# Optimization experiments

Hardware: AMD Instinct MI355X
Metric: run time of the kernel (lower is better)

Reference implementation:

```python
import jax, jax.numpy as jnp
import numpy as np

TAU_RC = 0.02
TAU_REF = 0.002
V_TH = 1.0
EPS = 1e-7


def lif_rate(I):
    # LIF firing-rate nonlinearity: r = 1/(tau_ref - tau_rc*log1p(-v_th/I)) for I > v_th+eps else 0
    good = I > V_TH + EPS
    safe_I = jnp.where(good, I, V_TH + 1.0)  # avoid log1p of invalid values
    r = 1.0 / (TAU_REF - TAU_RC * jnp.log1p(-V_TH / safe_I))
    return jnp.where(good, r, 0.0)


def setup_inputs() -> dict:
    key = jax.random.key(0)
    kq, kk, kv, ke, kg, kb = jax.random.split(key, 6)
    B, H, T, D = 2, 16, 2048, 64
    block_size = 2048
    Q = jax.random.normal(kq, (B, H, T, D), dtype=jnp.float32)
    K = jax.random.normal(kk, (B, H, T, D), dtype=jnp.float32)
    V = jax.random.normal(kv, (B, H, T, D), dtype=jnp.float32)
    enc = jax.random.normal(ke, (H, block_size, D), dtype=jnp.float32)
    # F.normalize(enc, dim=-1, eps=1e-8): x / max(||x||, eps)
    norm = jnp.maximum(jnp.linalg.norm(enc, axis=-1, keepdims=True), 1e-8)
    enc_hat = enc / norm
    gain = jax.random.uniform(kg, (1, H, block_size, 1), dtype=jnp.float32) * 200.0
    bias = jax.random.uniform(kb, (1, H, block_size, 1), dtype=jnp.float32)
    return {"Q": Q, "K": K, "V": V, "enc_hat": enc_hat, "gain": gain, "bias": bias}


def reference(Q, K, V, enc_hat, gain, bias):
    B, H, T, D = Q.shape
    temperature = jnp.asarray(D ** 0.5, dtype=Q.dtype)
    E = enc_hat[:, :T, :]          # [H, T, D]
    G = gain[:, :, :T, :]          # [1, H, T, 1]
    BIAS = bias[:, :, :T, :]       # [1, H, T, 1]
    # scores against fixed encoders (K is unused, matching the original module)
    I = G * jnp.einsum('bhtd,hsd->bhts', Q, E) + BIAS   # [B, H, T, T]
    scores = lif_rate(I) / temperature
    causal = jnp.tril(jnp.ones((T, T), dtype=bool))[None, None]
    scores = jnp.where(causal, scores, -jnp.inf)
    attn = jax.nn.softmax(scores, axis=-1)
    return jnp.einsum('bhts,bhsd->bhtd', attn, V)
```

## Files before the change

### kernel.cpp

```cpp
#include <hip/hip_runtime.h>
#include <hip/hip_bf16.h>
#include <math.h>

constexpr int Bb = 2, Hh = 16, Tt = 2048;

typedef __attribute__((ext_vector_type(8))) _Float16 f16x8;
typedef __attribute__((ext_vector_type(8))) short bf16x8;
typedef __attribute__((ext_vector_type(4))) float f32x4;
typedef __attribute__((ext_vector_type(16))) float f32x16;
typedef __attribute__((ext_vector_type(4))) unsigned int u32x4;
typedef unsigned int u32;

__device__ __forceinline__ short f2bf(float x){ __hip_bfloat16 h = __float2bfloat16(x); return *(short*)&h; }
__device__ __forceinline__ int swze(int row, int e){ return row*64 + ((((e>>3) ^ (row&7))<<3) | (e&7)); }
__device__ __forceinline__ int swzg(int row, int e0){ return row*64 + ((((e0>>3) ^ (row&7))<<3)); }

__device__ __forceinline__ void gll16(const void* g, void* l){
  __builtin_amdgcn_global_load_lds((const __attribute__((address_space(1))) u32*)g,
                                   (__attribute__((address_space(3))) u32*)l, 16, 0, 0);
}
__device__ __forceinline__ u32 cvtpk(float lo, float hi){
  u32 d; asm("v_cvt_pk_bf16_f32 %0, %1, %2" : "=v"(d) : "v"(lo), "v"(hi)); return d;
}

__global__ __launch_bounds__(256) void prep_e(const float* __restrict__ E, char* __restrict__ Eimg){
  const float* src = E + (size_t)blockIdx.x * 4096;
  char* dst = Eimg + (size_t)blockIdx.x * 16384;
#pragma unroll
  for (int i = 0; i < 2; ++i) {
    const int gid = threadIdx.x + 256 * i;
    const int row = gid >> 3, gc = gid & 7;
    const float* s8 = src + row * 64 + gc * 8;
    float4 a = *(const float4*)s8;
    float4 c = *(const float4*)(s8 + 4);
    float v[8] = {a.x, a.y, a.z, a.w, c.x, c.y, c.z, c.w};
    f16x8 hv, lv;
#pragma unroll
    for (int k = 0; k < 8; ++k) {
      _Float16 hi = (_Float16)v[k];
      hv[k] = hi; lv[k] = (_Float16)(v[k] - (float)hi);
    }
    const int off = row * 128 + ((gc ^ (row & 7)) << 4);
    *(f16x8*)(dst + off) = hv;
    *(f16x8*)(dst + 8192 + off) = lv;
  }
}

__global__ __launch_bounds__(256) void prep_v(const float* __restrict__ V, char* __restrict__ Vimg){
  __shared__ __align__(16) short Tl[64 * 64];
  const int tid = threadIdx.x;
  const int j = blockIdx.x & 31, bh = blockIdx.x >> 5;
  const int s0 = j * 64;
  {
    const int r = tid >> 2, c0 = (tid & 3) * 16;
    const float* src = V + ((size_t)bh * Tt + s0 + r) * 64 + c0;
#pragma unroll
    for (int i = 0; i < 4; ++i) {
      float4 t4 = ((const float4*)src)[i];
      float vv[4] = {t4.x, t4.y, t4.z, t4.w};
#pragma unroll
      for (int k = 0; k < 4; ++k) Tl[swze(c0 + 4 * i + k, r)] = f2bf(vv[k]);
    }
  }
  __syncthreads();
  {
    const int d = tid >> 2, sg = (tid & 3) * 16;
    bf16x8 a = *(const bf16x8*)&Tl[swzg(d, sg)];
    bf16x8 b = *(const bf16x8*)&Tl[swzg(d, sg + 8)];
    char* dst = Vimg + (size_t)blockIdx.x * 8192;
    *(bf16x8*)(dst + (sg >> 3) * 1024 + d * 16)       = a;
    *(bf16x8*)(dst + ((sg >> 3) + 1) * 1024 + d * 16) = b;
  }
}

__global__ __launch_bounds__(256, 3) void lif_attn15(
    const float* __restrict__ Q, const float* __restrict__ gain, const float* __restrict__ bias,
    const char* __restrict__ Eimg, const char* __restrict__ Vimg, float* __restrict__ out)
{
  __shared__ __align__(16) char Eb[2][16384];
  __shared__ __align__(16) float LsS[128];

  const int tid = threadIdx.x, lane = tid & 63;
  const int l31 = lane & 31, hi2 = lane >> 5;
  const int w = tid >> 6, wc = w & 1, wr = w >> 1;
  const int bh = blockIdx.x & 31, tb = 31 - (blockIdx.x >> 5);
  const int b = bh >> 4, h = bh & 15, t0 = tb * 64;
  const int tg = t0 + 32 * wc + l31;

  const char* etile = Eimg + (size_t)(h * 32) * 16384;
  const char* vtile = Vimg + (size_t)(bh * 32) * 8192;

  f16x8 qh[4], ql[4];
  {
    const float* qp = Q + ((size_t)(b * Hh + h) * Tt + tg) * 64 + 8 * hi2;
#pragma unroll
    for (int kk = 0; kk < 4; ++kk) {
      const float* p0 = qp + 16 * kk;
      float4 a = *(const float4*)p0;
      float4 c = *(const float4*)(p0 + 4);
      float v[8] = {a.x, a.y, a.z, a.w, c.x, c.y, c.z, c.w};
#pragma unroll
      for (int k = 0; k < 8; ++k) {
        _Float16 hi = (_Float16)v[k];
        qh[kk][k] = hi; ql[kk][k] = (_Float16)(v[k] - (float)hi);
      }
    }
  }
  const float gt = gain[h * Tt + tg], bt = bias[h * Tt + tg];

  const int rS = 32 * wr + l31;
  const int eB = rS * 128 + ((hi2 ^ (rS & 7)) << 4);

  const int g8a = 4 * wr + hi2;
  const char* vp0 = vtile + g8a * 1024 + l31 * 16;
  const char* vp1 = vtile + g8a * 1024 + (32 + l31) * 16;
  const char* vp2 = vtile + (g8a + 2) * 1024 + l31 * 16;
  const char* vp3 = vtile + (g8a + 2) * 1024 + (32 + l31) * 16;

  f32x16 oacc0 = 0.f, oacc1 = 0.f;
  float lsum = 0.f;
  f32x16 sA, sB;
  bf16x8 vA[4], vB[4];

  auto STAGE_E = [&](int n, int buf) {
    const char* g = etile + (size_t)n * 16384 + tid * 16;
    char* l = &Eb[buf][0] + tid * 16;
#pragma unroll
    for (int c2 = 0; c2 < 4; ++c2) gll16(g + c2 * 4096, l + c2 * 4096);
  };
  auto SSTEP = [&](int buf, f32x16& acc) {
    const char* ec = &Eb[buf][0];
    acc = 0.f;
#pragma unroll
    for (int kk = 0; kk < 4; ++kk) {
      f16x8 eh = *(const f16x8*)(ec + (eB ^ (kk << 5)));
      f16x8 el = *(const f16x8*)(ec + 8192 + (eB ^ (kk << 5)));
      acc = __builtin_amdgcn_mfma_f32_32x32x16_f16(eh, qh[kk], acc, 0, 0, 0);
      acc = __builtin_amdgcn_mfma_f32_32x32x16_f16(el, qh[kk], acc, 0, 0, 0);
      acc = __builtin_amdgcn_mfma_f32_32x32x16_f16(eh, ql[kk], acc, 0, 0, 0);
    }
  };
  auto VLOAD = [&](int n, bf16x8* vv) {
    const size_t o = (size_t)n * 8192;
    vv[0] = *(const bf16x8*)(vp0 + o);
    vv[1] = *(const bf16x8*)(vp1 + o);
    vv[2] = *(const bf16x8*)(vp2 + o);
    vv[3] = *(const bf16x8*)(vp3 + o);
  };

  auto BODY = [&](int j, f32x16& cur, f32x16& nxt, bf16x8* vc, bf16x8* vn) {
    if (j + 2 <= tb) STAGE_E(j + 2, j & 1);
    __builtin_amdgcn_sched_barrier(0);
    if (j + 1 <= tb) { SSTEP((j + 1) & 1, nxt); VLOAD(j + 1, vn); }
    float p[16];
#pragma unroll
    for (int r = 0; r < 16; ++r) {
      const float I = fmaf(gt, cur[r], bt);
      const float a = (I - 1.0f) * __builtin_fabsf(__builtin_amdgcn_rcpf(I));
      const float L2 = __log2f(a);
      const float den = fmaf(-0.013862944f, L2, 0.002f);
      const float rd = __builtin_amdgcn_rcpf(den);
      const float pv = __builtin_amdgcn_exp2f(fmaf(0.18033688f, rd, -90.169312f));
      p[r] = fmaxf(pv, 7.1892351e-28f);
    }
    if (j == tb) {
#pragma unroll
      for (int rq = 0; rq < 4; ++rq)
#pragma unroll
        for (int rr = 0; rr < 4; ++rr)
          if (32 * wr + 8 * rq + 4 * hi2 + rr > 32 * wc + l31) p[4 * rq + rr] = 0.f;
    }
#pragma unroll
    for (int r = 0; r < 16; ++r) lsum += p[r];
#pragma unroll
    for (int kp = 0; kp < 2; ++kp) {
      u32 x0 = cvtpk(p[8 * kp + 0], p[8 * kp + 1]);
      u32 x1 = cvtpk(p[8 * kp + 2], p[8 * kp + 3]);
      u32 y0 = cvtpk(p[8 * kp + 4], p[8 * kp + 5]);
      u32 y1 = cvtpk(p[8 * kp + 6], p[8 * kp + 7]);
      asm("v_permlane32_swap_b32 %0, %1" : "+v"(x0), "+v"(y0));
      asm("v_permlane32_swap_b32 %0, %1" : "+v"(x1), "+v"(y1));
      u32x4 af = {x0, x1, y0, y1};
      bf16x8 pa = *(bf16x8*)&af;
      oacc0 = __builtin_amdgcn_mfma_f32_32x32x16_bf16(pa, vc[2 * kp + 0], oacc0, 0, 0, 0);
      oacc1 = __builtin_amdgcn_mfma_f32_32x32x16_bf16(pa, vc[2 * kp + 1], oacc1, 0, 0, 0);
    }
  };

  STAGE_E(0, 0);
  if (tb >= 1) STAGE_E(1, 1);
  __builtin_amdgcn_sched_barrier(0);
  VLOAD(0, vA);
  asm volatile("s_waitcnt vmcnt(4)" ::: "memory");
  __builtin_amdgcn_s_barrier();
  __builtin_amdgcn_sched_barrier(0);
  SSTEP(0, sA);
  asm volatile("s_waitcnt vmcnt(4)" ::: "memory");
  __builtin_amdgcn_s_barrier();
  __builtin_amdgcn_sched_barrier(0);

  int j = 0;
  for (;;) {
    BODY(j, sA, sB, vA, vB);
    if (j == tb) break;
    asm volatile("s_waitcnt vmcnt(4)" ::: "memory");
    __builtin_amdgcn_s_barrier();
    __builtin_amdgcn_sched_barrier(0);
    ++j;
    BODY(j, sB, sA, vB, vA);
    if (j == tb) break;
    asm volatile("s_waitcnt vmcnt(4)" ::: "memory");
    __builtin_amdgcn_s_barrier();
    __builtin_amdgcn_sched_barrier(0);
    ++j;
  }

  lsum += __shfl_xor(lsum, 32);
  if (lane < 32) LsS[wr * 64 + wc * 32 + l31] = lsum;
  __syncthreads();
  float* red = (float*)&Eb[0][0];
  if (wr == 1) {
#pragma unroll
    for (int rq = 0; rq < 4; ++rq)
#pragma unroll
      for (int rr = 0; rr < 4; ++rr) {
        const int tr = 8 * rq + 4 * hi2 + rr;
        red[wc * 2048 + tr * 64 + l31]      = oacc0[4 * rq + rr];
        red[wc * 2048 + tr * 64 + 32 + l31] = oacc1[4 * rq + rr];
      }
  }
  __syncthreads();
  if (wr == 0) {
    float* ob = out + ((size_t)(b * Hh + h) * Tt + t0 + 32 * wc) * 64;
#pragma unroll
    for (int rq = 0; rq < 4; ++rq) {
      const int tr0 = 8 * rq + 4 * hi2;
      f32x4 lt0 = *(const f32x4*)&LsS[wc * 32 + tr0];
      f32x4 lt1 = *(const f32x4*)&LsS[64 + wc * 32 + tr0];
#pragma unroll
      for (int rr = 0; rr < 4; ++rr) {
        const int tr = tr0 + rr;
        const float linv = __builtin_amdgcn_rcpf(lt0[rr] + lt1[rr]);
        const float o0 = oacc0[4 * rq + rr] + red[wc * 2048 + tr * 64 + l31];
        const float o1 = oacc1[4 * rq + rr] + red[wc * 2048 + tr * 64 + 32 + l31];
        ob[(size_t)tr * 64 + l31]      = o0 * linv;
        ob[(size_t)tr * 64 + 32 + l31] = o1 * linv;
      }
    }
  }
}

extern "C" void kernel_launch(void* const* d_in, const int* in_sizes, int n_in,
                              void* d_out, int out_size, void* d_ws, size_t ws_size,
                              hipStream_t stream) {
  const float* Q    = (const float*)d_in[0];
  const float* V    = (const float*)d_in[2];
  const float* E    = (const float*)d_in[3];
  const float* gain = (const float*)d_in[4];
  const float* bias = (const float*)d_in[5];
  float* out = (float*)d_out;

  constexpr size_t EIMG_BYTES = (size_t)Hh * 32 * 16384;
  char* Eimg = (char*)d_ws;
  char* Vimg = (char*)d_ws + EIMG_BYTES;

  prep_e<<<Hh * 32, 256, 0, stream>>>(E, Eimg);
  prep_v<<<Bb * Hh * 32, 256, 0, stream>>>(V, Vimg);
  lif_attn15<<<1024, 256, 0, stream>>>(Q, gain, bias, Eimg, Vimg, out);
}
```

Baseline: 72.39 us.

## Split long causal rows across blocks to balance work, then merge partials

Adds a load-balanced causal attention kernel. Each of the 1024 blocks now handles either a long query tile's first 16 key tiles (writing partial output and row sums to workspace), or a pair made of that long tile's remaining key tiles plus a short query tile. A finalize kernel then adds the partials and normalises. This evens out per-block work under the triangular causal mask, at the cost of an extra kernel launch, extra global traffic for partials, and a fallback when the workspace is too small.

Result: slower. 136.0 us (+87.9%).

```diff
diff --git a/kernel.cpp b/kernel.cpp
--- a/kernel.cpp
+++ b/kernel.cpp
@@ -73,6 +73,231 @@
   }
 }
 
+__global__ __launch_bounds__(256, 3) void lif_attn16(
+    const float* __restrict__ Q, const float* __restrict__ gain, const float* __restrict__ bias,
+    const char* __restrict__ Eimg, const char* __restrict__ Vimg, float* __restrict__ out,
+    float* __restrict__ wsAO, float* __restrict__ wsAL, float* __restrict__ wsBL)
+{
+  __shared__ __align__(16) char Eb[2][16384];
+  __shared__ __align__(16) float LsS[128];
+
+  const int tid = threadIdx.x, lane = tid & 63;
+  const int l31 = lane & 31, hi2 = lane >> 5;
+  const int w = tid >> 6, wc = w & 1, wr = w >> 1;
+  const int bh = blockIdx.x & 31;
+  const int m  = blockIdx.x >> 5;
+  const int p  = m & 15, isB = m >> 4;
+  const int b = bh >> 4, h = bh & 15;
+
+  const char* etile = Eimg + (size_t)(h * 32) * 16384;
+  const char* vtile = Vimg + (size_t)(bh * 32) * 8192;
+
+  const int rS = 32 * wr + l31;
+  const int eB = rS * 128 + ((hi2 ^ (rS & 7)) << 4);
+  const int g8a = 4 * wr + hi2;
+  const char* vp0 = vtile + g8a * 1024 + l31 * 16;
+  const char* vp1 = vtile + g8a * 1024 + (32 + l31) * 16;
+  const char* vp2 = vtile + (g8a + 2) * 1024 + l31 * 16;
+  const char* vp3 = vtile + (g8a + 2) * 1024 + (32 + l31) * 16;
+
+  const int nph = 1 + isB;
+  for (int ph = 0; ph < nph; ++ph) {
+    const int tb   = ph ? p : (31 - p);
+    const int jlo  = (isB && ph == 0) ? 16 : 0;
+    const int jhi  = isB ? tb : 15;
+    const int mode = isB ? (ph == 0 ? 1 : 0) : 2;
+    const int t0 = tb * 64;
+    const int tg = t0 + 32 * wc + l31;
+
+    f16x8 qh[4], ql[4];
+    {
+      const float* qp = Q + ((size_t)(b * Hh + h) * Tt + tg) * 64 + 8 * hi2;
+#pragma unroll
+      for (int kk = 0; kk < 4; ++kk) {
+        const float* p0 = qp + 16 * kk;
+        float4 a = *(const float4*)p0;
+        float4 c = *(const float4*)(p0 + 4);
+        float v[8] = {a.x, a.y, a.z, a.w, c.x, c.y, c.z, c.w};
+#pragma unroll
+        for (int k = 0; k < 8; ++k) {
+          _Float16 hi = (_Float16)v[k];
+          qh[kk][k] = hi; ql[kk][k] = (_Float16)(v[k] - (float)hi);
+        }
+      }
+    }
+    const float gt = gain[h * Tt + tg], bt = bias[h * Tt + tg];
+
+    f32x16 oacc0 = 0.f, oacc1 = 0.f;
+    float lsum = 0.f;
+    f32x16 sA, sB;
+    bf16x8 vA[4], vB[4];
+
+    auto STAGE_E = [&](int n) {
+      const char* g = etile + (size_t)n * 16384 + tid * 16;
+      char* l = &Eb[n & 1][0] + tid * 16;
+#pragma unroll
+      for (int c2 = 0; c2 < 4; ++c2) gll16(g + c2 * 4096, l + c2 * 4096);
+    };
+    auto SSTEP = [&](int n, f32x16& acc) {
+      const char* ec = &Eb[n & 1][0];
+      acc = 0.f;
+#pragma unroll
+      for (int kk = 0; kk < 4; ++kk) {
+        f16x8 eh = *(const f16x8*)(ec + (eB ^ (kk << 5)));
+        f16x8 el = *(const f16x8*)(ec + 8192 + (eB ^ (kk << 5)));
+        acc = __builtin_amdgcn_mfma_f32_32x32x16_f16(eh, qh[kk], acc, 0, 0, 0);
+        acc = __builtin_amdgcn_mfma_f32_32x32x16_f16(el, qh[kk], acc, 0, 0, 0);
+        acc = __builtin_amdgcn_mfma_f32_32x32x16_f16(eh, ql[kk], acc, 0, 0, 0);
+      }
+    };
+    auto VLOAD = [&](int n, bf16x8* vv) {
+      const size_t o = (size_t)n * 8192;
+      vv[0] = *(const bf16x8*)(vp0 + o);
+      vv[1] = *(const bf16x8*)(vp1 + o);
+      vv[2] = *(const bf16x8*)(vp2 + o);
+      vv[3] = *(const bf16x8*)(vp3 + o);
+    };
+
+    auto BODY = [&](int j, f32x16& cur, f32x16& nxt, bf16x8* vc, bf16x8* vn) {
+      if (j + 2 <= jhi) STAGE_E(j + 2);
+      __builtin_amdgcn_sched_barrier(0);
+      if (j + 1 <= jhi) { SSTEP(j + 1, nxt); VLOAD(j + 1, vn); }
+      float pp[16];
+#pragma unroll
+      for (int r = 0; r < 16; ++r) {
+        const float I = fmaf(gt, cur[r], bt);
+        const float a = (I - 1.0f) * __builtin_fabsf(__builtin_amdgcn_rcpf(I));
+        const float L2 = __log2f(a);
+        const float den = fmaf(-0.013862944f, L2, 0.002f);
+        const float rd = __builtin_amdgcn_rcpf(den);
+        const float pv = __builtin_amdgcn_exp2f(fmaf(0.18033688f, rd, -90.169312f));
+        pp[r] = fmaxf(pv, 7.1892351e-28f);
+      }
+      if (j == tb) {
+#pragma unroll
+        for (int rq = 0; rq < 4; ++rq)
+#pragma unroll
+          for (int rr = 0; rr < 4; ++rr)
+            if (32 * wr + 8 * rq + 4 * hi2 + rr > 32 * wc + l31) pp[4 * rq + rr] = 0.f;
+      }
+#pragma unroll
+      for (int r = 0; r < 16; ++r) lsum += pp[r];
+#pragma unroll
+      for (int kp = 0; kp < 2; ++kp) {
+        u32 x0 = cvtpk(pp[8 * kp + 0], pp[8 * kp + 1]);
+        u32 x1 = cvtpk(pp[8 * kp + 2], pp[8 * kp + 3]);
+        u32 y0 = cvtpk(pp[8 * kp + 4], pp[8 * kp + 5]);
+        u32 y1 = cvtpk(pp[8 * kp + 6], pp[8 * kp + 7]);
+        asm("v_permlane32_swap_b32 %0, %1" : "+v"(x0), "+v"(y0));
+        asm("v_permlane32_swap_b32 %0, %1" : "+v"(x1), "+v"(y1));
+        u32x4 af = {x0, x1, y0, y1};
+        bf16x8 pa = *(bf16x8*)&af;
+        oacc0 = __builtin_amdgcn_mfma_f32_32x32x16_bf16(pa, vc[2 * kp + 0], oacc0, 0, 0, 0);
+        oacc1 = __builtin_amdgcn_mfma_f32_32x32x16_bf16(pa, vc[2 * kp + 1], oacc1, 0, 0, 0);
+      }
+    };
+
+    STAGE_E(jlo);
+    if (jlo + 1 <= jhi) STAGE_E(jlo + 1);
+    __builtin_amdgcn_sched_barrier(0);
+    VLOAD(jlo, vA);
+    asm volatile("s_waitcnt vmcnt(4)" ::: "memory");
+    __builtin_amdgcn_s_barrier();
+    __builtin_amdgcn_sched_barrier(0);
+    SSTEP(jlo, sA);
+    asm volatile("s_waitcnt vmcnt(4)" ::: "memory");
+    __builtin_amdgcn_s_barrier();
+    __builtin_amdgcn_sched_barrier(0);
+
+    int j = jlo;
+    for (;;) {
+      BODY(j, sA, sB, vA, vB);
+      if (j == jhi) break;
+      asm volatile("s_waitcnt vmcnt(4)" ::: "memory");
+      __builtin_amdgcn_s_barrier();
+      __builtin_amdgcn_sched_barrier(0);
+      ++j;
+      BODY(j, sB, sA, vB, vA);
+      if (j == jhi) break;
+      asm volatile("s_waitcnt vmcnt(4)" ::: "memory");
+      __builtin_amdgcn_s_barrier();
+      __builtin_amdgcn_sched_barrier(0);
+      ++j;
+    }
+
+    lsum += __shfl_xor(lsum, 32);
+    if (lane < 32) LsS[wr * 64 + wc * 32 + l31] = lsum;
+    __syncthreads();
+    float* red = (float*)&Eb[0][0];
+    if (wr == 1) {
+#pragma unroll
+      for (int rq = 0; rq < 4; ++rq)
+#pragma unroll
+        for (int rr = 0; rr < 4; ++rr) {
+          const int tr = 8 * rq + 4 * hi2 + rr;
+          red[wc * 2048 + tr * 64 + l31]      = oacc0[4 * rq + rr];
+          red[wc * 2048 + tr * 64 + 32 + l31] = oacc1[4 * rq + rr];
+        }
+    }
+    __syncthreads();
+    if (wr == 0) {
+      float* ob = out + ((size_t)(b * Hh + h) * Tt + t0 + 32 * wc) * 64;
+      float* ab = wsAO + (size_t)(bh * 16 + p) * 4096 + (size_t)(32 * wc) * 64;
+      float* lb = (mode == 1 ? wsBL : wsAL) + (size_t)(bh * 16 + p) * 64 + 32 * wc;
+#pragma unroll
+      for (int rq = 0; rq < 4; ++rq) {
+        const int tr0 = 8 * rq + 4 * hi2;
+        f32x4 lt0 = *(const f32x4*)&LsS[wc * 32 + tr0];
+        f32x4 lt1 = *(const f32x4*)&LsS[64 + wc * 32 + tr0];
+#pragma unroll
+        for (int rr = 0; rr < 4; ++rr) {
+          const int tr = tr0 + rr;
+          const float lt = lt0[rr] + lt1[rr];
+          const float o0 = oacc0[4 * rq + rr] + red[wc * 2048 + tr * 64 + l31];
+          const float o1 = oacc1[4 * rq + rr] + red[wc * 2048 + tr * 64 + 32 + l31];
+          if (mode == 0) {
+            const float linv = __builtin_amdgcn_rcpf(lt);
+            ob[(size_t)tr * 64 + l31]      = o0 * linv;
+            ob[(size_t)tr * 64 + 32 + l31] = o1 * linv;
+          } else if (mode == 1) {
+            ob[(size_t)tr * 64 + l31]      = o0;
+            ob[(size_t)tr * 64 + 32 + l31] = o1;
+            if (l31 == 0) lb[tr] = lt;
+          } else {
+            ab[(size_t)tr * 64 + l31]      = o0;
+            ab[(size_t)tr * 64 + 32 + l31] = o1;
+            if (l31 == 0) lb[tr] = lt;
+          }
+        }
+      }
+    }
+    __syncthreads();
+  }
+}
+
+__global__ __launch_bounds__(256) void finalize_split(
+    float* __restrict__ out, const float* __restrict__ wsAO,
+    const float* __restrict__ wsAL, const float* __restrict__ wsBL)
+{
+  const int bid = blockIdx.x;
+  const int bh = bid >> 4, p = bid & 15;
+  const int tb = 31 - p, t0 = tb * 64;
+  const int tid = threadIdx.x;
+  const int r = tid >> 2, c0 = (tid & 3) * 16;
+  const float l = wsAL[(size_t)(bh * 16 + p) * 64 + r] + wsBL[(size_t)(bh * 16 + p) * 64 + r];
+  const float linv = __builtin_amdgcn_rcpf(l);
+  float* orow = out + ((size_t)bh * Tt + t0 + r) * 64 + c0;
+  const float* arow = wsAO + (size_t)(bh * 16 + p) * 4096 + (size_t)r * 64 + c0;
+#pragma unroll
+  for (int i = 0; i < 4; ++i) {
+    float4 o = ((float4*)orow)[i];
+    float4 a = ((const float4*)arow)[i];
+    o.x = (o.x + a.x) * linv; o.y = (o.y + a.y) * linv;
+    o.z = (o.z + a.z) * linv; o.w = (o.w + a.w) * linv;
+    ((float4*)orow)[i] = o;
+  }
+}
+
 __global__ __launch_bounds__(256, 3) void lif_attn15(
     const float* __restrict__ Q, const float* __restrict__ gain, const float* __restrict__ bias,
     const char* __restrict__ Eimg, const char* __restrict__ Vimg, float* __restrict__ out)
@@ -107,10 +332,8 @@
     }
   }
   const float gt = gain[h * Tt + tg], bt = bias[h * Tt + tg];
-
   const int rS = 32 * wr + l31;
   const int eB = rS * 128 + ((hi2 ^ (rS & 7)) << 4);
-
   const int g8a = 4 * wr + hi2;
   const char* vp0 = vtile + g8a * 1024 + l31 * 16;
   const char* vp1 = vtile + g8a * 1024 + (32 + l31) * 16;
@@ -147,7 +370,6 @@
     vv[2] = *(const bf16x8*)(vp2 + o);
     vv[3] = *(const bf16x8*)(vp3 + o);
   };
-
   auto BODY = [&](int j, f32x16& cur, f32x16& nxt, bf16x8* vc, bf16x8* vn) {
     if (j + 2 <= tb) STAGE_E(j + 2, j & 1);
     __builtin_amdgcn_sched_barrier(0);
@@ -260,11 +482,24 @@
   const float* bias = (const float*)d_in[5];
   float* out = (float*)d_out;
 
-  constexpr size_t EIMG_BYTES = (size_t)Hh * 32 * 16384;
+  constexpr size_t EIMG = (size_t)Hh * 32 * 16384;
+  constexpr size_t VIMG = (size_t)Bb * Hh * 32 * 8192;
+  constexpr size_t AO   = (size_t)32 * 16 * 4096 * 4;
+  constexpr size_t AL   = (size_t)32 * 16 * 64 * 4;
+  constexpr size_t NEED = EIMG + VIMG + AO + 2 * AL;
+
   char* Eimg = (char*)d_ws;
-  char* Vimg = (char*)d_ws + EIMG_BYTES;
-
+  char* Vimg = (char*)d_ws + EIMG;
   prep_e<<<Hh * 32, 256, 0, stream>>>(E, Eimg);
   prep_v<<<Bb * Hh * 32, 256, 0, stream>>>(V, Vimg);
-  lif_attn15<<<1024, 256, 0, stream>>>(Q, gain, bias, Eimg, Vimg, out);
-}
+
+  if (ws_size >= NEED) {
+    float* wsAO = (float*)((char*)d_ws + EIMG + VIMG);
+    float* wsAL = (float*)((char*)d_ws + EIMG + VIMG + AO);
+    float* wsBL = (float*)((char*)d_ws + EIMG + VIMG + AO + AL);
+    lif_attn16<<<1024, 256, 0, stream>>>(Q, gain, bias, Eimg, Vimg, out, wsAO, wsAL, wsBL);
+    finalize_split<<<512, 256, 0, stream>>>(out, wsAO, wsAL, wsBL);
+  } else {
+    lif_attn15<<<1024, 256, 0, stream>>>(Q, gain, bias, Eimg, Vimg, out);
+  }
+}
```
